# Performance work log

Measured on AMD Instinct MI355X. Metric: run time of the kernel, lower is better.

## Reference

```python
import jax, jax.numpy as jnp
import numpy as np

N = 50000   # nodes
E = 800000  # edges (no self loops; conv adds them)
F = 64      # in_channels == out_channels
P = 6       # pos dim (pos_nn MLP input = 6)
H = 64      # hidden width of pos_nn / attn_nn


def _mlp(x, W1, b1, W2, b2):
    # PyG MLP([a, 64, b], norm=None, plain_last=False): ReLU after both layers
    return jax.nn.relu(jax.nn.relu(x @ W1 + b1) @ W2 + b2)


def setup_inputs() -> dict:
    key = jax.random.key(0)
    ks = jax.random.split(key, 16)

    def w(k, shape, fan_in):
        return jax.random.normal(k, shape, jnp.float32) / np.sqrt(fan_in)

    src = jax.random.randint(ks[0], (E,), 0, N)
    dst = jax.random.randint(ks[1], (E,), 0, N)
    src = jnp.where(src == dst, (src + 1) % N, src)  # no pre-existing self loops
    edge_index = jnp.stack([src, dst]).astype(jnp.int32)

    return dict(
        x=jax.random.normal(ks[2], (N, F), jnp.float32),
        pos=jax.random.normal(ks[3], (N, P), jnp.float32),
        edge_index=edge_index,
        W_in=w(ks[4], (F, F), F), b_in=jnp.zeros((F,), jnp.float32),
        W_out=w(ks[5], (F, F), F), b_out=jnp.zeros((F,), jnp.float32),
        W_lin=w(ks[6], (F, F), F),   # conv value proj, bias=False
        W_src=w(ks[7], (F, F), F),   # lin_src, bias=False
        W_dst=w(ks[8], (F, F), F),   # lin_dst, bias=False
        Wp1=w(ks[9], (P, H), P), bp1=jnp.zeros((H,), jnp.float32),
        Wp2=w(ks[10], (H, F), H), bp2=jnp.zeros((F,), jnp.float32),
        Wa1=w(ks[11], (F, H), F), ba1=jnp.zeros((H,), jnp.float32),
        Wa2=w(ks[12], (H, F), H), ba2=jnp.zeros((F,), jnp.float32),
    )


def reference(x, pos, edge_index, W_in, b_in, W_out, b_out, W_lin, W_src, W_dst,
              Wp1, bp1, Wp2, bp2, Wa1, ba1, Wa2, ba2):
    residual = jax.lax.stop_gradient(x)  # residual = x.clone().detach()
    h = jax.nn.relu(x @ W_in + b_in)

    # PointTransformerConv
    a_src = h @ W_src
    a_dst = h @ W_dst
    v = h @ W_lin

    loop = jnp.arange(N, dtype=edge_index.dtype)  # add_self_loops=True
    src = jnp.concatenate([edge_index[0], loop])
    dst = jnp.concatenate([edge_index[1], loop])

    delta = _mlp(pos[dst] - pos[src], Wp1, bp1, Wp2, bp2)        # pos_nn(pos_i - pos_j)
    alpha = _mlp(a_dst[dst] - a_src[src] + delta, Wa1, ba1, Wa2, ba2)

    # scatter-softmax over destination neighborhoods (per channel)
    m = jax.ops.segment_max(alpha, dst, num_segments=N)
    e = jnp.exp(alpha - m[dst])
    s = jax.ops.segment_sum(e, dst, num_segments=N)
    wgt = e / (s[dst] + 1e-16)

    msg = wgt * (v[src] + delta)
    out = jax.ops.segment_sum(msg, dst, num_segments=N)

    out = jax.nn.relu(out @ W_out + b_out)
    return out + residual
```

## Files before the change

### kernel.cpp

```cpp
#include <hip/hip_runtime.h>

#define NN 50000
#define NE 800000
#define ETOT (NE + NN)
#define NB ((NN + 255) / 256)

typedef _Float16 f16;
typedef _Float16 v8h __attribute__((ext_vector_type(8)));
typedef float v4f __attribute__((ext_vector_type(4)));

__device__ __forceinline__ float bcast(float v, int lane) {
  return __int_as_float(__builtin_amdgcn_readlane(__float_as_int(v), lane));
}

__device__ __forceinline__ int fr_off(int kb, int nb, int q, int p) {
  return (((nb * 2 + kb) * 4 + q) * 16 + p) * 8;
}


__global__ __launch_bounds__(256) void k_setup(
    const float* __restrict__ W_in, const float* __restrict__ W_src,
    const float* __restrict__ W_dst, const float* __restrict__ W_lin,
    const float* __restrict__ W_out, const float* __restrict__ Wp2,
    const float* __restrict__ Wa1, const float* __restrict__ Wa2,
    const float* __restrict__ Wp1, f16* __restrict__ FR,
    const int* __restrict__ edst, int* __restrict__ deg) {
  const int t = blockIdx.x * 256 + threadIdx.x;
  if (t < NE) atomicAdd(&deg[edst[t]], 1);
  if (t < 8 * 4096) {
    const float* Ws[8] = {W_in, W_src, W_dst, W_lin, W_out, Wp2, Wa1, Wa2};
    const int m = t >> 12, idx = t & 4095;
    const int i = idx & 7, p = (idx >> 3) & 15, q = (idx >> 7) & 3;
    const int kb = (idx >> 9) & 1, nb = (idx >> 10) & 3;
    FR[t] = (f16)Ws[m][(kb * 32 + q * 8 + i) * 64 + nb * 16 + p];
  } else if (t < 8 * 4096 + 2048) {
    const int idx = t - 8 * 4096;
    const int i = idx & 7, p = (idx >> 3) & 15, q = (idx >> 7) & 3, nb = idx >> 9;
    const int k = q * 8 + i;
    FR[t] = (k < 6) ? (f16)Wp1[k * 64 + nb * 16 + p] : (f16)0.f;
  }
}


__global__ __launch_bounds__(256) void k_scan1(const int* __restrict__ deg,
                                               int* __restrict__ bsum) {
  __shared__ int ws[4];
  const int t = threadIdx.x, b = blockIdx.x;
  const int i = b * 256 + t;
  int s = (i < NN) ? (deg[i] + 1) : 0;
#pragma unroll
  for (int d = 1; d < 64; d <<= 1) s += __shfl_xor(s, d, 64);
  if ((t & 63) == 0) ws[t >> 6] = s;
  __syncthreads();
  if (t == 0) bsum[b] = ws[0] + ws[1] + ws[2] + ws[3];
}

__global__ __launch_bounds__(256) void k_scan2(const int* __restrict__ bsum,
                                               int* __restrict__ bpre,
                                               int* __restrict__ offsets) {
  __shared__ int ws[4];
  const int t = threadIdx.x, lane = t & 63, w = t >> 6;
  int v = (t < NB) ? bsum[t] : 0;
  int x = v;
#pragma unroll
  for (int d = 1; d < 64; d <<= 1) {
    int y = __shfl_up(x, d, 64);
    if (lane >= d) x += y;
  }
  if (lane == 63) ws[w] = x;
  __syncthreads();
  if (t == 0) {
    int c = 0;
#pragma unroll
    for (int j = 0; j < 4; ++j) { int tmp = ws[j]; ws[j] = c; c += tmp; }
    offsets[NN] = c;
  }
  __syncthreads();
  if (t < NB) bpre[t] = ws[w] + x - v;
}

__global__ __launch_bounds__(256) void k_scan3(
    const int* __restrict__ deg, const int* __restrict__ bpre,
    int* __restrict__ offsets, int* __restrict__ ssrc, int* __restrict__ cursor) {
  __shared__ int ws[4], wpre[4];
  const int t = threadIdx.x, b = blockIdx.x, lane = t & 63, w = t >> 6;
  const int i = b * 256 + t;
  int v = (i < NN) ? (deg[i] + 1) : 0;
  int x = v;
#pragma unroll
  for (int d = 1; d < 64; d <<= 1) {
    int y = __shfl_up(x, d, 64);
    if (lane >= d) x += y;
  }
  if (lane == 63) ws[w] = x;
  __syncthreads();
  if (t == 0) {
    int c = 0;
#pragma unroll
    for (int j = 0; j < 4; ++j) { wpre[j] = c; c += ws[j]; }
  }
  __syncthreads();
  if (i < NN) {
    const int off = bpre[b] + wpre[w] + x - v;
    offsets[i] = off;
    ssrc[off] = i;
    cursor[i] = off + 1;
  }
}

__global__ void k_scatter(const int* __restrict__ src, const int* __restrict__ dst,
                          int* __restrict__ cursor, int* __restrict__ ssrc) {
  int e = blockIdx.x * 256 + threadIdx.x;
  if (e < NE) {
    int p = atomicAdd(&cursor[dst[e]], 1);
    ssrc[p] = src[e];
  }
}


__global__ __launch_bounds__(256, 2) void k_node(
    const float* __restrict__ x, const float* __restrict__ pos,
    const float* __restrict__ b_in, const f16* __restrict__ FR,
    f16* __restrict__ adsth, f16* __restrict__ vh,
    f16* __restrict__ asrch, f16* __restrict__ Qh) {
  __shared__ f16 lds[4][16 * 72];
  const int lane = threadIdx.x & 63, w = threadIdx.x >> 6;
  const int q = lane >> 4, p = lane & 15;
  const int base = (blockIdx.x * 4 + w) * 16;
  if (base >= NN) return;
  const f16* FWin = FR;
  const f16* FWsrc = FR + 1 * 4096;
  const f16* FWdst = FR + 2 * 4096;
  const f16* FWlin = FR + 3 * 4096;
  const f16* FWp1 = FR + 8 * 4096;

  v8h xa[2];
#pragma unroll
  for (int kb = 0; kb < 2; ++kb) {
    const float4 f0 = *(const float4*)(x + (base + p) * 64 + kb * 32 + q * 8);
    const float4 f1 = *(const float4*)(x + (base + p) * 64 + kb * 32 + q * 8 + 4);
    v8h a;
    a[0] = (f16)f0.x; a[1] = (f16)f0.y; a[2] = (f16)f0.z; a[3] = (f16)f0.w;
    a[4] = (f16)f1.x; a[5] = (f16)f1.y; a[6] = (f16)f1.z; a[7] = (f16)f1.w;
    xa[kb] = a;
  }
#pragma unroll
  for (int nb = 0; nb < 4; ++nb) {
    v4f c = {0.f, 0.f, 0.f, 0.f};
    c = __builtin_amdgcn_mfma_f32_16x16x32_f16(xa[0], *(const v8h*)&FWin[fr_off(0, nb, q, p)], c, 0, 0, 0);
    c = __builtin_amdgcn_mfma_f32_16x16x32_f16(xa[1], *(const v8h*)&FWin[fr_off(1, nb, q, p)], c, 0, 0, 0);
    const float bi = b_in[p + 16 * nb];
#pragma unroll
    for (int r = 0; r < 4; ++r)
      lds[w][(q * 4 + r) * 72 + p + 16 * nb] = (f16)fmaxf(c[r] + bi, 0.f);
  }
  v8h hA[2];
#pragma unroll
  for (int kb = 0; kb < 2; ++kb)
    hA[kb] = *(const v8h*)&lds[w][p * 72 + kb * 32 + q * 8];

#pragma unroll
  for (int nb = 0; nb < 4; ++nb) {
    v4f c = {0.f, 0.f, 0.f, 0.f};
    c = __builtin_amdgcn_mfma_f32_16x16x32_f16(hA[0], *(const v8h*)&FWsrc[fr_off(0, nb, q, p)], c, 0, 0, 0);
    c = __builtin_amdgcn_mfma_f32_16x16x32_f16(hA[1], *(const v8h*)&FWsrc[fr_off(1, nb, q, p)], c, 0, 0, 0);
#pragma unroll
    for (int r = 0; r < 4; ++r)
      asrch[(base + q * 4 + r) * 64 + p + 16 * nb] = (f16)c[r];
  }
#pragma unroll
  for (int nb = 0; nb < 4; ++nb) {
    v4f c = {0.f, 0.f, 0.f, 0.f};
    c = __builtin_amdgcn_mfma_f32_16x16x32_f16(hA[0], *(const v8h*)&FWdst[fr_off(0, nb, q, p)], c, 0, 0, 0);
    c = __builtin_amdgcn_mfma_f32_16x16x32_f16(hA[1], *(const v8h*)&FWdst[fr_off(1, nb, q, p)], c, 0, 0, 0);
#pragma unroll
    for (int r = 0; r < 4; ++r)
      adsth[(base + q * 4 + r) * 64 + p + 16 * nb] = (f16)c[r];
  }
#pragma unroll
  for (int nb = 0; nb < 4; ++nb) {
    v4f c = {0.f, 0.f, 0.f, 0.f};
    c = __builtin_amdgcn_mfma_f32_16x16x32_f16(hA[0], *(const v8h*)&FWlin[fr_off(0, nb, q, p)], c, 0, 0, 0);
    c = __builtin_amdgcn_mfma_f32_16x16x32_f16(hA[1], *(const v8h*)&FWlin[fr_off(1, nb, q, p)], c, 0, 0, 0);
#pragma unroll
    for (int r = 0; r < 4; ++r)
      vh[(base + q * 4 + r) * 64 + p + 16 * nb] = (f16)c[r];
  }
  v8h pa;
#pragma unroll
  for (int i = 0; i < 8; ++i) {
    const int k = q * 8 + i;
    pa[i] = (k < 6) ? (f16)pos[(base + p) * 6 + k] : (f16)0.f;
  }
#pragma unroll
  for (int nb = 0; nb < 4; ++nb) {
    const v8h b = *(const v8h*)&FWp1[(((nb * 4 + q) * 16) + p) * 8];
    v4f c = {0.f, 0.f, 0.f, 0.f};
    c = __builtin_amdgcn_mfma_f32_16x16x32_f16(pa, b, c, 0, 0, 0);
#pragma unroll
    for (int r = 0; r < 4; ++r)
      Qh[(base + q * 4 + r) * 64 + p + 16 * nb] = (f16)c[r];
  }
}


__global__ __launch_bounds__(256, 3) void k_conv(
    const f16* __restrict__ Qh, const float* __restrict__ bp1,
    const f16* __restrict__ FRconv,
    const float* __restrict__ bp2, const float* __restrict__ ba1,
    const float* __restrict__ ba2,
    const f16* __restrict__ asrch, const f16* __restrict__ adsth,
    const f16* __restrict__ vh,
    const int* __restrict__ offsets, const int* __restrict__ ssrc,
    const float* __restrict__ W_out, const float* __restrict__ b_out,
    const float* __restrict__ x, float* __restrict__ out) {
  __shared__ f16 wfr[12288];
  __shared__ f16 tbufD[4][16 * 72];
  __shared__ f16 tbufH[4][16 * 72];
  __shared__ f16 stashQ[4][64];
  __shared__ f16 stashA[4][64];
  __shared__ float bias[192];
  const int t = threadIdx.x;
#pragma unroll
  for (int it = 0; it < 6; ++it)
    *(uint4*)&wfr[(it * 256 + t) * 8] = *(const uint4*)&FRconv[(it * 256 + t) * 8];
  if (t < 192) bias[t] = (t < 64) ? bp2[t] : (t < 128 ? ba1[t - 64] : ba2[t - 128]);

  const int lane = t & 63, w = t >> 6;
  const int q = lane >> 4, p = lane & 15;
  const int n = blockIdx.x * 4 + w;

  stashQ[w][lane] = (f16)((float)Qh[n * 64 + lane] + bp1[lane]);
  stashA[w][lane] = adsth[n * 64 + lane];
  __syncthreads();

  const int e0 = __builtin_amdgcn_readfirstlane(offsets[n]);
  const int e1 = __builtin_amdgcn_readfirstlane(offsets[n + 1]);
  const int cnt = e1 - e0;

  float m_[4], s_[4], ac_[4];
#pragma unroll
  for (int nb = 0; nb < 4; ++nb) { m_[nb] = 0.f; s_[nb] = 0.f; ac_[nb] = 0.f; }

  for (int cb = 0; cb < cnt; cb += 16) {
    const int jA = ssrc[e0 + min(cb + p, cnt - 1)];
    int jC[4]; bool okC[4];
#pragma unroll
    for (int r = 0; r < 4; ++r) {
      const int tt = cb + q * 4 + r;
      okC[r] = tt < cnt;
      jC[r] = ssrc[e0 + min(tt, cnt - 1)];
    }
    v8h uA[2];
#pragma unroll
    for (int kb = 0; kb < 2; ++kb) {
      const v8h qi = *(const v8h*)&stashQ[w][kb * 32 + q * 8];
      const v8h qj = *(const v8h*)(Qh + jA * 64 + kb * 32 + q * 8);
      v8h a;
#pragma unroll
      for (int i = 0; i < 8; ++i) {
        const f16 d = qi[i] - qj[i];
        a[i] = d > (f16)0 ? d : (f16)0;
      }
      uA[kb] = a;
    }
    unsigned z0;
    asm volatile("v_mov_b32 %0, 0" : "=v"(z0));
#pragma unroll
    for (int nb = 0; nb < 4; ++nb) {
      v4f c = {0.f, 0.f, 0.f, 0.f};
      c = __builtin_amdgcn_mfma_f32_16x16x32_f16(uA[0], *(const v8h*)&wfr[z0 + fr_off(0, nb, q, p)], c, 0, 0, 0);
      c = __builtin_amdgcn_mfma_f32_16x16x32_f16(uA[1], *(const v8h*)&wfr[z0 + fr_off(1, nb, q, p)], c, 0, 0, 0);
      const float bp2c = bias[p + 16 * nb];
#pragma unroll
      for (int r = 0; r < 4; ++r)
        tbufD[w][(q * 4 + r) * 72 + p + 16 * nb] = (f16)fmaxf(c[r] + bp2c, 0.f);
    }
#pragma unroll
    for (int kb = 0; kb < 2; ++kb) {
      const v8h adc = *(const v8h*)&stashA[w][kb * 32 + q * 8];
      const v8h dj = *(const v8h*)&tbufD[w][p * 72 + kb * 32 + q * 8];
      const v8h aj = *(const v8h*)(asrch + jA * 64 + kb * 32 + q * 8);
      uA[kb] = (adc - aj) + dj;
    }
    unsigned z1;
    asm volatile("v_mov_b32 %0, 4096" : "=v"(z1));
#pragma unroll
    for (int nb = 0; nb < 4; ++nb) {
      v4f c = {0.f, 0.f, 0.f, 0.f};
      c = __builtin_amdgcn_mfma_f32_16x16x32_f16(uA[0], *(const v8h*)&wfr[z1 + fr_off(0, nb, q, p)], c, 0, 0, 0);
      c = __builtin_amdgcn_mfma_f32_16x16x32_f16(uA[1], *(const v8h*)&wfr[z1 + fr_off(1, nb, q, p)], c, 0, 0, 0);
      const float ba1c = bias[64 + p + 16 * nb];
#pragma unroll
      for (int r = 0; r < 4; ++r)
        tbufH[w][(q * 4 + r) * 72 + p + 16 * nb] = (f16)fmaxf(c[r] + ba1c, 0.f);
    }
#pragma unroll
    for (int kb = 0; kb < 2; ++kb)
      uA[kb] = *(const v8h*)&tbufH[w][p * 72 + kb * 32 + q * 8];
    unsigned z2;
    asm volatile("v_mov_b32 %0, 8192" : "=v"(z2));
#pragma unroll
    for (int nb = 0; nb < 4; ++nb) {
      v4f c = {0.f, 0.f, 0.f, 0.f};
      c = __builtin_amdgcn_mfma_f32_16x16x32_f16(uA[0], *(const v8h*)&wfr[z2 + fr_off(0, nb, q, p)], c, 0, 0, 0);
      c = __builtin_amdgcn_mfma_f32_16x16x32_f16(uA[1], *(const v8h*)&wfr[z2 + fr_off(1, nb, q, p)], c, 0, 0, 0);
      const float ba2c = bias[128 + p + 16 * nb];
      float al[4];
#pragma unroll
      for (int r = 0; r < 4; ++r)
        al[r] = okC[r] ? fmaxf(c[r] + ba2c, 0.f) : -3.0e38f;
      float mn = m_[nb];
#pragma unroll
      for (int r = 0; r < 4; ++r) mn = fmaxf(mn, al[r]);
      const float sc = __expf(m_[nb] - mn);
      float ss = s_[nb] * sc;
      float aa = ac_[nb] * sc;
#pragma unroll
      for (int r = 0; r < 4; ++r) {
        const float wv = __expf(al[r] - mn);
        const float vj = (float)vh[jC[r] * 64 + p + 16 * nb];
        const float dC = (float)tbufD[w][(q * 4 + r) * 72 + p + 16 * nb];
        ss += wv;
        aa = fmaf(wv, vj + dC, aa);
      }
      m_[nb] = mn; s_[nb] = ss; ac_[nb] = aa;
    }
  }
#pragma unroll
  for (int st = 16; st <= 32; st <<= 1) {
#pragma unroll
    for (int nb = 0; nb < 4; ++nb) {
      const float mo = __shfl_xor(m_[nb], st, 64);
      const float so = __shfl_xor(s_[nb], st, 64);
      const float ao = __shfl_xor(ac_[nb], st, 64);
      const float mn = fmaxf(m_[nb], mo);
      const float c1 = __expf(m_[nb] - mn), c2 = __expf(mo - mn);
      s_[nb] = s_[nb] * c1 + so * c2;
      ac_[nb] = ac_[nb] * c1 + ao * c2;
      m_[nb] = mn;
    }
  }
  const float o = ac_[q] / (s_[q] + 1e-16f);
  float a0 = b_out[lane], a1 = 0.f, a2 = 0.f, a3 = 0.f;
#pragma unroll
  for (int k = 0; k < 64; k += 4) {
    a0 = fmaf(bcast(o, k + 0), W_out[(k + 0) * 64 + lane], a0);
    a1 = fmaf(bcast(o, k + 1), W_out[(k + 1) * 64 + lane], a1);
    a2 = fmaf(bcast(o, k + 2), W_out[(k + 2) * 64 + lane], a2);
    a3 = fmaf(bcast(o, k + 3), W_out[(k + 3) * 64 + lane], a3);
  }
  out[n * 64 + lane] = fmaxf((a0 + a1) + (a2 + a3), 0.f) + x[n * 64 + lane];
}


extern "C" void kernel_launch(void* const* d_in, const int* in_sizes, int n_in,
                              void* d_out, int out_size, void* d_ws, size_t ws_size,
                              hipStream_t stream) {
  const float* x     = (const float*)d_in[0];
  const float* pos   = (const float*)d_in[1];
  const int*   ei    = (const int*)d_in[2];
  const float* W_in  = (const float*)d_in[3];
  const float* b_in  = (const float*)d_in[4];
  const float* W_out = (const float*)d_in[5];
  const float* b_out = (const float*)d_in[6];
  const float* W_lin = (const float*)d_in[7];
  const float* W_src = (const float*)d_in[8];
  const float* W_dst = (const float*)d_in[9];
  const float* Wp1   = (const float*)d_in[10];
  const float* bp1   = (const float*)d_in[11];
  const float* Wp2   = (const float*)d_in[12];
  const float* bp2   = (const float*)d_in[13];
  const float* Wa1   = (const float*)d_in[14];
  const float* ba1   = (const float*)d_in[15];
  const float* Wa2   = (const float*)d_in[16];
  const float* ba2   = (const float*)d_in[17];

  f16*  Qh     = (f16*)d_ws;
  f16*  asrch  = Qh + NN * 64;
  f16*  adsth  = asrch + NN * 64;
  f16*  vh     = adsth + NN * 64;
  f16*  FR     = vh + NN * 64;
  int*  deg    = (int*)(FR + 8 * 4096 + 2048);
  int* offsets = deg + NN;
  int* cursor  = offsets + NN + 1;
  int* bsum    = cursor + NN;
  int* bpre    = bsum + NB;
  int* ssrc    = bpre + NB;

  const int* esrc = ei;
  const int* edst = ei + NE;

  hipMemsetAsync(deg, 0, NN * sizeof(int), stream);
  k_setup<<<(NE + 255) / 256, 256, 0, stream>>>(
      W_in, W_src, W_dst, W_lin, W_out, Wp2, Wa1, Wa2, Wp1, FR, edst, deg);
  k_node<<<(NN / 16 + 3) / 4, 256, 0, stream>>>(x, pos, b_in, FR, adsth, vh, asrch, Qh);
  k_scan1<<<NB, 256, 0, stream>>>(deg, bsum);
  k_scan2<<<1, 256, 0, stream>>>(bsum, bpre, offsets);
  k_scan3<<<NB, 256, 0, stream>>>(deg, bpre, offsets, ssrc, cursor);
  k_scatter<<<(NE + 255) / 256, 256, 0, stream>>>(esrc, edst, cursor, ssrc);
  k_conv<<<NN / 4, 256, 0, stream>>>(Qh, bp1, FR + 5 * 4096, bp2, ba1, ba2,
                                     asrch, adsth, vh, offsets, ssrc,
                                     W_out, b_out, x, (float*)d_out);
}
```

Measured before the change: 340.1 us.

## Gather source values row-wise via LDS, drop online softmax max, widen blocks

The value rows v[src] are now loaded as contiguous 16-byte vectors alongside the Qh and a_src rows. They are transposed through the tbufH shared buffer once it is free, replacing four scattered per-element gathers per lane. The online-softmax running max and its rescaling are removed, so exp is applied to alpha directly. This relies on alpha (a ReLU output) staying small enough not to overflow. Blocks now handle 8 nodes with 512 threads, so the shared weight-fragment load is spread over twice as many nodes, at the cost of a larger LDS footprint per block.

Measured after the change: 322.6 us. -5.1%, faster.

```diff
diff --git a/kernel.cpp b/kernel.cpp
--- a/kernel.cpp
+++ b/kernel.cpp
@@ -204,7 +204,7 @@
 }
 
 
-__global__ __launch_bounds__(256, 3) void k_conv(
+__global__ __launch_bounds__(512, 4) void k_conv(
     const f16* __restrict__ Qh, const float* __restrict__ bp1,
     const f16* __restrict__ FRconv,
     const float* __restrict__ bp2, const float* __restrict__ ba1,
@@ -215,20 +215,20 @@
     const float* __restrict__ W_out, const float* __restrict__ b_out,
     const float* __restrict__ x, float* __restrict__ out) {
   __shared__ f16 wfr[12288];
-  __shared__ f16 tbufD[4][16 * 72];
-  __shared__ f16 tbufH[4][16 * 72];
-  __shared__ f16 stashQ[4][64];
-  __shared__ f16 stashA[4][64];
+  __shared__ f16 tbufD[8][16 * 72];
+  __shared__ f16 tbufH[8][16 * 72];
+  __shared__ f16 stashQ[8][64];
+  __shared__ f16 stashA[8][64];
   __shared__ float bias[192];
   const int t = threadIdx.x;
 #pragma unroll
-  for (int it = 0; it < 6; ++it)
-    *(uint4*)&wfr[(it * 256 + t) * 8] = *(const uint4*)&FRconv[(it * 256 + t) * 8];
+  for (int it = 0; it < 3; ++it)
+    *(uint4*)&wfr[(it * 512 + t) * 8] = *(const uint4*)&FRconv[(it * 512 + t) * 8];
   if (t < 192) bias[t] = (t < 64) ? bp2[t] : (t < 128 ? ba1[t - 64] : ba2[t - 128]);
 
   const int lane = t & 63, w = t >> 6;
   const int q = lane >> 4, p = lane & 15;
-  const int n = blockIdx.x * 4 + w;
+  const int n = blockIdx.x * 8 + w;
 
   stashQ[w][lane] = (f16)((float)Qh[n * 64 + lane] + bp1[lane]);
   stashA[w][lane] = adsth[n * 64 + lane];
@@ -238,28 +238,27 @@
   const int e1 = __builtin_amdgcn_readfirstlane(offsets[n + 1]);
   const int cnt = e1 - e0;
 
-  float m_[4], s_[4], ac_[4];
-#pragma unroll
-  for (int nb = 0; nb < 4; ++nb) { m_[nb] = 0.f; s_[nb] = 0.f; ac_[nb] = 0.f; }
+  float s_[4], ac_[4];
+#pragma unroll
+  for (int nb = 0; nb < 4; ++nb) { s_[nb] = 0.f; ac_[nb] = 0.f; }
 
   for (int cb = 0; cb < cnt; cb += 16) {
     const int jA = ssrc[e0 + min(cb + p, cnt - 1)];
-    int jC[4]; bool okC[4];
-#pragma unroll
-    for (int r = 0; r < 4; ++r) {
-      const int tt = cb + q * 4 + r;
-      okC[r] = tt < cnt;
-      jC[r] = ssrc[e0 + min(tt, cnt - 1)];
+    v8h qj[2], aj[2], vA[2];
+#pragma unroll
+    for (int kb = 0; kb < 2; ++kb) {
+      qj[kb] = *(const v8h*)(Qh + jA * 64 + kb * 32 + q * 8);
+      aj[kb] = *(const v8h*)(asrch + jA * 64 + kb * 32 + q * 8);
+      vA[kb] = *(const v8h*)(vh + jA * 64 + kb * 32 + q * 8);
     }
     v8h uA[2];
 #pragma unroll
     for (int kb = 0; kb < 2; ++kb) {
       const v8h qi = *(const v8h*)&stashQ[w][kb * 32 + q * 8];
-      const v8h qj = *(const v8h*)(Qh + jA * 64 + kb * 32 + q * 8);
       v8h a;
 #pragma unroll
       for (int i = 0; i < 8; ++i) {
-        const f16 d = qi[i] - qj[i];
+        const f16 d = qi[i] - qj[kb][i];
         a[i] = d > (f16)0 ? d : (f16)0;
       }
       uA[kb] = a;
@@ -280,8 +279,7 @@
     for (int kb = 0; kb < 2; ++kb) {
       const v8h adc = *(const v8h*)&stashA[w][kb * 32 + q * 8];
       const v8h dj = *(const v8h*)&tbufD[w][p * 72 + kb * 32 + q * 8];
-      const v8h aj = *(const v8h*)(asrch + jA * 64 + kb * 32 + q * 8);
-      uA[kb] = (adc - aj) + dj;
+      uA[kb] = (adc - aj[kb]) + dj;
     }
     unsigned z1;
     asm volatile("v_mov_b32 %0, 4096" : "=v"(z1));
@@ -298,6 +296,9 @@
 #pragma unroll
     for (int kb = 0; kb < 2; ++kb)
       uA[kb] = *(const v8h*)&tbufH[w][p * 72 + kb * 32 + q * 8];
+#pragma unroll
+    for (int kb = 0; kb < 2; ++kb)
+      *(v8h*)&tbufH[w][p * 72 + kb * 32 + q * 8] = vA[kb];
     unsigned z2;
     asm volatile("v_mov_b32 %0, 8192" : "=v"(z2));
 #pragma unroll
@@ -306,39 +307,24 @@
       c = __builtin_amdgcn_mfma_f32_16x16x32_f16(uA[0], *(const v8h*)&wfr[z2 + fr_off(0, nb, q, p)], c, 0, 0, 0);
       c = __builtin_amdgcn_mfma_f32_16x16x32_f16(uA[1], *(const v8h*)&wfr[z2 + fr_off(1, nb, q, p)], c, 0, 0, 0);
       const float ba2c = bias[128 + p + 16 * nb];
-      float al[4];
-#pragma unroll
-      for (int r = 0; r < 4; ++r)
-        al[r] = okC[r] ? fmaxf(c[r] + ba2c, 0.f) : -3.0e38f;
-      float mn = m_[nb];
-#pragma unroll
-      for (int r = 0; r < 4; ++r) mn = fmaxf(mn, al[r]);
-      const float sc = __expf(m_[nb] - mn);
-      float ss = s_[nb] * sc;
-      float aa = ac_[nb] * sc;
 #pragma unroll
       for (int r = 0; r < 4; ++r) {
-        const float wv = __expf(al[r] - mn);
-        const float vj = (float)vh[jC[r] * 64 + p + 16 * nb];
+        const bool ok = (cb + q * 4 + r) < cnt;
+        const float al = ok ? fmaxf(c[r] + ba2c, 0.f) : -3.0e38f;
+        const float wv = __expf(al);
+        const float vj = (float)tbufH[w][(q * 4 + r) * 72 + p + 16 * nb];
         const float dC = (float)tbufD[w][(q * 4 + r) * 72 + p + 16 * nb];
-        ss += wv;
-        aa = fmaf(wv, vj + dC, aa);
+        s_[nb] += wv;
+        ac_[nb] = fmaf(wv, vj + dC, ac_[nb]);
       }
-      m_[nb] = mn; s_[nb] = ss; ac_[nb] = aa;
     }
   }
 #pragma unroll
   for (int st = 16; st <= 32; st <<= 1) {
 #pragma unroll
     for (int nb = 0; nb < 4; ++nb) {
-      const float mo = __shfl_xor(m_[nb], st, 64);
-      const float so = __shfl_xor(s_[nb], st, 64);
-      const float ao = __shfl_xor(ac_[nb], st, 64);
-      const float mn = fmaxf(m_[nb], mo);
-      const float c1 = __expf(m_[nb] - mn), c2 = __expf(mo - mn);
-      s_[nb] = s_[nb] * c1 + so * c2;
-      ac_[nb] = ac_[nb] * c1 + ao * c2;
-      m_[nb] = mn;
+      s_[nb] += __shfl_xor(s_[nb], st, 64);
+      ac_[nb] += __shfl_xor(ac_[nb], st, 64);
     }
   }
   const float o = ac_[q] / (s_[q] + 1e-16f);
@@ -399,7 +385,7 @@
   k_scan2<<<1, 256, 0, stream>>>(bsum, bpre, offsets);
   k_scan3<<<NB, 256, 0, stream>>>(deg, bpre, offsets, ssrc, cursor);
   k_scatter<<<(NE + 255) / 256, 256, 0, stream>>>(esrc, edst, cursor, ssrc);
-  k_conv<<<NN / 4, 256, 0, stream>>>(Qh, bp1, FR + 5 * 4096, bp2, ba1, ba2,
+  k_conv<<<NN / 8, 512, 0, stream>>>(Qh, bp1, FR + 5 * 4096, bp2, ba1, ba2,
                                      asrch, adsth, vh, offsets, ssrc,
                                      W_out, b_out, x, (float*)d_out);
 }
```
